# Optimization experiments

Measured on AMD Instinct MI355X. Metric: run time of the kernel, lower is better.

The kernel has to match this reference:

```python
import jax, jax.numpy as jnp
import numpy as np

NUM_EMBED = 1024
EMBED_DIM = 256
DECAY = 0.99
EPS = 1e-05
COMMIT = 0.25


def setup_inputs() -> dict:
    key = jax.random.key(0)
    k1, k2, k3 = jax.random.split(key, 3)
    z = jax.random.normal(k1, (64, 32, 32, EMBED_DIM), dtype=jnp.float32)
    lim = 1.0 / NUM_EMBED
    embeddings = jax.random.uniform(k2, (NUM_EMBED, EMBED_DIM), minval=-lim, maxval=lim, dtype=jnp.float32)
    ema_embed = jax.random.uniform(k3, (NUM_EMBED, EMBED_DIM), minval=-lim, maxval=lim, dtype=jnp.float32)
    cluster_size = jnp.zeros((NUM_EMBED,), dtype=jnp.float32)
    return {"z": z, "embeddings": embeddings, "ema_embed": ema_embed, "cluster_size": cluster_size}


def reference(z, embeddings, ema_embed, cluster_size):
    B, H, W, D = z.shape
    zf = z.reshape(-1, D)  # [N, D]
    # squared euclidean distances to codebook: [N, K]
    distances = (zf ** 2).sum(-1, keepdims=True) + (embeddings ** 2).sum(-1) - 2.0 * (zf @ embeddings.T)
    closest = jnp.argmin(distances, axis=-1)  # [N] int
    quantized_indices = closest.reshape(B, H, W)[:, None]  # [B,1,H,W]
    quantized = embeddings[closest].reshape(z.shape)  # gather instead of one-hot GEMM

    # --- training-mode EMA codebook update (buffer math, no grads) ---
    n_i = jnp.zeros((NUM_EMBED,), dtype=zf.dtype).at[closest].add(1.0)  # per-code counts
    new_cluster = cluster_size * DECAY + n_i * (1.0 - DECAY)
    dw = jnp.zeros_like(embeddings).at[closest].add(zf)  # scatter-add of assigned vectors
    new_ema = ema_embed * DECAY + dw * (1.0 - DECAY)
    n = new_cluster.sum()
    new_cluster = (new_cluster + EPS) / (n + NUM_EMBED * EPS) * n
    new_embeddings = new_ema / new_cluster[:, None]

    commitment_loss = jnp.mean((quantized - z) ** 2)
    st_quantized = z + jax.lax.stop_gradient(quantized - z)  # straight-through
    loss = commitment_loss * COMMIT
    return loss, st_quantized, quantized_indices, new_embeddings, new_cluster, new_ema
```

## Files before the change

kernel.cpp:

```cpp
#include <hip/hip_runtime.h>
#include <float.h>
#include <stdint.h>

#define K_EMB 1024
#define D_EMB 256

typedef _Float16 half8 __attribute__((ext_vector_type(8)));
typedef float f32x4_t __attribute__((ext_vector_type(4)));


__global__ void convert_e_kernel(const float* __restrict__ e, _Float16* __restrict__ ehp,
                                 float* __restrict__ t2, unsigned int* __restrict__ flag_cnt) {
  if (blockIdx.x == 0 && threadIdx.x == 0) { flag_cnt[0] = 0; flag_cnt[1] = 0; }
  int row = blockIdx.x * 4 + (threadIdx.x >> 6);
  int lane = threadIdx.x & 63;
  float4 v = ((const float4*)(e + (size_t)row * D_EMB))[lane];
  float s = v.x * v.x + v.y * v.y + v.z * v.z + v.w * v.w;
#pragma unroll
  for (int off = 32; off > 0; off >>= 1) s += __shfl_down(s, off, 64);
  if (lane == 0) t2[row] = s;
  _Float16* dst = ehp + (size_t)row * D_EMB + lane * 4;
  dst[0] = (_Float16)v.x; dst[1] = (_Float16)v.y;
  dst[2] = (_Float16)v.z; dst[3] = (_Float16)v.w;
}


#define BM 256
#define CCH 64
#define NCH (K_EMB / CCH)
#define DELTA 1.5e-4f

__launch_bounds__(512, 2)
__global__ void argmin_mfma_kernel(const float* __restrict__ z,
                                   const _Float16* __restrict__ eh,
                                   const float* __restrict__ t2,
                                   int* __restrict__ closest,
                                   float* __restrict__ idx_out,
                                   unsigned int* __restrict__ flag_cnt,
                                   unsigned int* __restrict__ flag_row,
                                   unsigned int* __restrict__ flag_cand) {
  __shared__ _Float16 ebuf[CCH * D_EMB];
  const int tid = threadIdx.x;
  const int wid = tid >> 6;
  const int lane = tid & 63;
  const int c = lane & 15, g = lane >> 4;
  const int row0 = blockIdx.x * BM + wid * 32;

  half8 A[2][8];
#pragma unroll
  for (int fr = 0; fr < 2; ++fr)
#pragma unroll
    for (int df = 0; df < 8; ++df) {
      const float* zp = z + (size_t)(row0 + fr * 16 + c) * D_EMB + df * 32 + g * 8;
      const float4 v0 = *(const float4*)zp;
      const float4 v1 = *(const float4*)(zp + 4);
      half8 h;
      h[0] = (_Float16)v0.x; h[1] = (_Float16)v0.y; h[2] = (_Float16)v0.z; h[3] = (_Float16)v0.w;
      h[4] = (_Float16)v1.x; h[5] = (_Float16)v1.y; h[6] = (_Float16)v1.z; h[7] = (_Float16)v1.w;
      A[fr][df] = h;
    }

  float m1[8], m2[8], m3[8];
  int k1[8], k2[8];
#pragma unroll
  for (int s = 0; s < 8; ++s) { m1[s] = FLT_MAX; m2[s] = FLT_MAX; m3[s] = FLT_MAX; k1[s] = 0; k2[s] = 0; }

#define INS(s, dvv, kkv)                                        \
  {                                                             \
    const float dv_ = (dvv); const int kk_ = (kkv);             \
    const bool lt1 = dv_ < m1[s], lt2 = dv_ < m2[s], lt3 = dv_ < m3[s]; \
    m3[s] = lt2 ? m2[s] : (lt3 ? dv_ : m3[s]);                  \
    m2[s] = lt1 ? m1[s] : (lt2 ? dv_ : m2[s]);                  \
    k2[s] = lt1 ? k1[s] : (lt2 ? kk_ : k2[s]);                  \
    m1[s] = lt1 ? dv_ : m1[s];                                  \
    k1[s] = lt1 ? kk_ : k1[s];                                  \
  }

  const int scode = tid >> 3;
  const int s8 = tid & 7;
  const int swz_w = (scode & 7) << 3;
  const int rswz = (c & 7) << 3;

  for (int cb = 0; cb < NCH; ++cb) {
    __syncthreads();
    {
      const _Float16* src = eh + (size_t)(cb * CCH + scode) * D_EMB + s8 * 32;
      _Float16* dst = ebuf + scode * D_EMB;
#pragma unroll
      for (int u = 0; u < 4; ++u) {
        int elem = s8 * 32 + u * 8;
        *(half8*)(dst + (elem ^ swz_w)) = *(const half8*)(src + u * 8);
      }
    }
    __syncthreads();

    f32x4_t acc[2][4];
#pragma unroll
    for (int fr = 0; fr < 2; ++fr)
#pragma unroll
      for (int fc = 0; fc < 4; ++fc) acc[fr][fc] = (f32x4_t){0.f, 0.f, 0.f, 0.f};

#pragma unroll
    for (int d = 0; d < 8; ++d) {
      half8 Bh[4];
#pragma unroll
      for (int fc = 0; fc < 4; ++fc) {
        const int elem = (d * 32 + g * 8) ^ rswz;
        Bh[fc] = *(const half8*)(ebuf + (fc * 16 + c) * D_EMB + elem);
      }
#pragma unroll
      for (int fr = 0; fr < 2; ++fr)
#pragma unroll
        for (int fc = 0; fc < 4; ++fc)
          acc[fr][fc] = __builtin_amdgcn_mfma_f32_16x16x32_f16(A[fr][d], Bh[fc], acc[fr][fc], 0, 0, 0);
    }

#pragma unroll
    for (int fc = 0; fc < 4; ++fc) {
      const int kk = cb * CCH + fc * 16 + c;
      const float t2c = t2[kk];
#pragma unroll
      for (int fr = 0; fr < 2; ++fr)
#pragma unroll
        for (int r = 0; r < 4; ++r) {
          const float dv = fmaf(-2.f, acc[fr][fc][r], t2c);
          const int s = fr * 4 + r;
          INS(s, dv, kk)
        }
    }
  }

#pragma unroll
  for (int m = 1; m <= 8; m <<= 1) {
#pragma unroll
    for (int s = 0; s < 8; ++s) {
      const float om1 = __shfl_xor(m1[s], m, 64);
      const int ok1 = __shfl_xor(k1[s], m, 64);
      const float om2 = __shfl_xor(m2[s], m, 64);
      const int ok2 = __shfl_xor(k2[s], m, 64);
      const float om3 = __shfl_xor(m3[s], m, 64);
      INS(s, om1, ok1)
      INS(s, om2, ok2)
      m3[s] = fminf(m3[s], om3);
    }
  }
#undef INS

  if (c == 0) {
#pragma unroll
    for (int s = 0; s < 8; ++s) {
      const int fr = s >> 2, r = s & 3;
      const int row = row0 + fr * 16 + g * 4 + r;
      closest[row] = k1[s];
      idx_out[row] = (float)k1[s];
      if (m2[s] - m1[s] < DELTA) {
        const unsigned int p = atomicAdd(flag_cnt, 1u);
        flag_row[p] = (unsigned int)row;
        flag_cand[p] = (unsigned int)k1[s] | ((unsigned int)k2[s] << 10) |
                       ((m3[s] - m1[s] < DELTA) ? (1u << 20) : 0u);
      }
    }
  }
}


__launch_bounds__(256, 4)
__global__ void fixup_pair_kernel(const float* __restrict__ z, const float* __restrict__ emb,
                                  const float* __restrict__ t2,
                                  const unsigned int* __restrict__ flag_cnt,
                                  const unsigned int* __restrict__ flag_row,
                                  const unsigned int* __restrict__ flag_cand,
                                  int* __restrict__ closest, float* __restrict__ idx_out,
                                  unsigned int* __restrict__ flag2_cnt,
                                  unsigned int* __restrict__ flag2) {
  const int tid = threadIdx.x;
  const int q = tid & 3;
  const unsigned int cnt = *flag_cnt;
  const unsigned int nquads = (gridDim.x * 256) >> 2;
  for (unsigned int i = (blockIdx.x * 256 + tid) >> 2; i < cnt; i += nquads) {
    const int row = (int)flag_row[i];
    const unsigned int cand = flag_cand[i];
    if ((cand >> 20) & 1u) {
      if (q == 0) {
        const unsigned int p = atomicAdd(flag2_cnt, 1u);
        flag2[p] = (unsigned int)row;
      }
      continue;
    }
    const int ka = (int)(cand & 1023u), kb = (int)((cand >> 10) & 1023u);
    const float4* zp = (const float4*)(z + (size_t)row * D_EMB) + q * 16;
    const float4* ap = (const float4*)(emb + (size_t)ka * D_EMB) + q * 16;
    const float4* bp = (const float4*)(emb + (size_t)kb * D_EMB) + q * 16;
    float s0 = 0.f, sa = 0.f, sb = 0.f;
#pragma unroll 8
    for (int u = 0; u < 16; ++u) {
      const float4 zv = zp[u], av = ap[u], bv = bp[u];
      s0 = fmaf(zv.x, zv.x, s0); s0 = fmaf(zv.y, zv.y, s0);
      s0 = fmaf(zv.z, zv.z, s0); s0 = fmaf(zv.w, zv.w, s0);
      sa = fmaf(zv.x, av.x, sa); sa = fmaf(zv.y, av.y, sa);
      sa = fmaf(zv.z, av.z, sa); sa = fmaf(zv.w, av.w, sa);
      sb = fmaf(zv.x, bv.x, sb); sb = fmaf(zv.y, bv.y, sb);
      sb = fmaf(zv.z, bv.z, sb); sb = fmaf(zv.w, bv.w, sb);
    }
#pragma unroll
    for (int m = 1; m <= 2; m <<= 1) {
      s0 += __shfl_xor(s0, m, 64);
      sa += __shfl_xor(sa, m, 64);
      sb += __shfl_xor(sb, m, 64);
    }
    if (q == 0) {
      const float da = (s0 + t2[ka]) - 2.f * sa;
      const float db = (s0 + t2[kb]) - 2.f * sb;
      int kbest = ka;
      if (db < da || (db == da && kb < ka)) kbest = kb;
      closest[row] = kbest;
      idx_out[row] = (float)kbest;
    }
  }
}


__launch_bounds__(256, 4)
__global__ void fixup_full_kernel(const float* __restrict__ z, const float* __restrict__ emb,
                                  const float* __restrict__ t2,
                                  const unsigned int* __restrict__ flag2_cnt,
                                  const unsigned int* __restrict__ flag2,
                                  int* __restrict__ closest, float* __restrict__ idx_out) {
  __shared__ float zs[D_EMB];
  __shared__ float t1s;
  __shared__ float redm[4];
  __shared__ int redk[4];
  const int tid = threadIdx.x;
  const int lane = tid & 63, wv = tid >> 6;
  const unsigned int cnt = *flag2_cnt;
  for (unsigned int j = blockIdx.x; j < cnt; j += gridDim.x) {
    __syncthreads();
    const int row = (int)flag2[j];
    if (wv == 0) {
      const float4 v = ((const float4*)(z + (size_t)row * D_EMB))[lane];
      ((float4*)zs)[lane] = v;
      float s = v.x * v.x + v.y * v.y + v.z * v.z + v.w * v.w;
#pragma unroll
      for (int off = 32; off > 0; off >>= 1) s += __shfl_down(s, off, 64);
      if (lane == 0) t1s = s;
    }
    __syncthreads();
    const float4* e0 = (const float4*)(emb + (size_t)(4 * tid + 0) * D_EMB);
    const float4* e1 = (const float4*)(emb + (size_t)(4 * tid + 1) * D_EMB);
    const float4* e2 = (const float4*)(emb + (size_t)(4 * tid + 2) * D_EMB);
    const float4* e3 = (const float4*)(emb + (size_t)(4 * tid + 3) * D_EMB);
    const float4* zp4 = (const float4*)zs;
    float a0 = 0.f, a1 = 0.f, a2 = 0.f, a3 = 0.f;
    for (int i = 0; i < 64; ++i) {
      const float4 z4 = zp4[i];
      const float4 v0 = e0[i], v1 = e1[i], v2 = e2[i], v3 = e3[i];
      a0 = fmaf(z4.x, v0.x, a0); a0 = fmaf(z4.y, v0.y, a0);
      a0 = fmaf(z4.z, v0.z, a0); a0 = fmaf(z4.w, v0.w, a0);
      a1 = fmaf(z4.x, v1.x, a1); a1 = fmaf(z4.y, v1.y, a1);
      a1 = fmaf(z4.z, v1.z, a1); a1 = fmaf(z4.w, v1.w, a1);
      a2 = fmaf(z4.x, v2.x, a2); a2 = fmaf(z4.y, v2.y, a2);
      a2 = fmaf(z4.z, v2.z, a2); a2 = fmaf(z4.w, v2.w, a2);
      a3 = fmaf(z4.x, v3.x, a3); a3 = fmaf(z4.y, v3.y, a3);
      a3 = fmaf(z4.z, v3.z, a3); a3 = fmaf(z4.w, v3.w, a3);
    }
    const float t1v = t1s;
    float best = FLT_MAX;
    int bk = 0x7fffffff;
    const float dvs[4] = {(t1v + t2[4 * tid + 0]) - 2.f * a0,
                          (t1v + t2[4 * tid + 1]) - 2.f * a1,
                          (t1v + t2[4 * tid + 2]) - 2.f * a2,
                          (t1v + t2[4 * tid + 3]) - 2.f * a3};
#pragma unroll
    for (int cc = 0; cc < 4; ++cc) {
      const int k = 4 * tid + cc;
      if (dvs[cc] < best) { best = dvs[cc]; bk = k; }
    }
#pragma unroll
    for (int m = 1; m <= 32; m <<= 1) {
      const float ob = __shfl_xor(best, m, 64);
      const int ok = __shfl_xor(bk, m, 64);
      if (ob < best || (ob == best && ok < bk)) { best = ob; bk = ok; }
    }
    if (lane == 0) { redm[wv] = best; redk[wv] = bk; }
    __syncthreads();
    if (tid == 0) {
      float b = redm[0];
      int k = redk[0];
#pragma unroll
      for (int w = 1; w < 4; ++w)
        if (redm[w] < b || (redm[w] == b && redk[w] < k)) { b = redm[w]; k = redk[w]; }
      closest[row] = k;
      idx_out[row] = (float)k;
    }
  }
}


__global__ void hist1_kernel(const int* __restrict__ closest, unsigned int* __restrict__ rank,
                             unsigned int* __restrict__ blockhist) {
  __shared__ unsigned int lh[K_EMB];
  const int t = threadIdx.x;
  lh[t] = 0;
  __syncthreads();
  const int row = blockIdx.x * 1024 + t;
  rank[row] = atomicAdd(&lh[closest[row]], 1u);
  __syncthreads();
  blockhist[blockIdx.x * K_EMB + t] = lh[t];
}

__global__ void hist2_kernel(unsigned int* __restrict__ blockhist, const float* __restrict__ cs,
                             unsigned int* __restrict__ base, float* __restrict__ newc,
                             float* __restrict__ o_ncl, int nblocks) {
  __shared__ unsigned int sc[K_EMB];
  __shared__ float fr[K_EMB];
  const int bin = threadIdx.x;
  unsigned int s = 0;
  for (int b = 0; b < nblocks; ++b) {
    const unsigned int v = blockhist[b * K_EMB + bin];
    blockhist[b * K_EMB + bin] = s;
    s += v;
  }
  sc[bin] = s;
  __syncthreads();
  for (int off = 1; off < K_EMB; off <<= 1) {
    const unsigned int t = (bin >= off) ? sc[bin - off] : 0u;
    __syncthreads();
    sc[bin] += t;
    __syncthreads();
  }
  base[bin] = sc[bin] - s;
  const float pre = cs[bin] * 0.99f + (float)s * (float)(1.0 - 0.99);
  fr[bin] = pre;
  __syncthreads();
  for (int st = 512; st > 0; st >>= 1) {
    if (bin < st) fr[bin] += fr[bin + st];
    __syncthreads();
  }
  const float n = fr[0];
  const float ncl = (pre + 1e-5f) / (n + (float)(K_EMB * 1e-5)) * n;
  newc[bin] = ncl;
  o_ncl[bin] = ncl;
}

__global__ void hist3_kernel(const int* __restrict__ closest, const unsigned int* __restrict__ rank,
                             const unsigned int* __restrict__ blockhist,
                             const unsigned int* __restrict__ base,
                             unsigned int* __restrict__ sorted) {
  const int t = threadIdx.x;
  const int row = blockIdx.x * 1024 + t;
  const int k = closest[row];
  sorted[base[k] + blockhist[blockIdx.x * K_EMB + k] + rank[row]] = (unsigned int)row;
}


__global__ void dwsum_kernel(const float* __restrict__ z, const unsigned int* __restrict__ sorted,
                             const unsigned int* __restrict__ base, const float* __restrict__ ema,
                             const float* __restrict__ newc, const float* __restrict__ emb,
                             float* __restrict__ o_st, float* __restrict__ o_nema,
                             float* __restrict__ o_nemb, float* __restrict__ loss_part, int N) {
  const int k = blockIdx.x;
  const int lane = threadIdx.x & 63, wv = threadIdx.x >> 6;
  const unsigned int b0 = base[k];
  const unsigned int b1 = (k == K_EMB - 1) ? (unsigned int)N : base[k + 1];
  const float4 ev = ((const float4*)(emb + (size_t)k * D_EMB))[lane];
  float4 acc = {0.f, 0.f, 0.f, 0.f};
  float ls = 0.f;
  for (unsigned int j = b0 + wv; j < b1; j += 4) {
    const unsigned int row = sorted[j];
    const float4 zv = ((const float4*)(z + (size_t)row * D_EMB))[lane];
    const float dx = ev.x - zv.x, dy = ev.y - zv.y, dz = ev.z - zv.z, dww = ev.w - zv.w;
    float* sp = o_st + (size_t)row * D_EMB + lane * 4;
    sp[0] = zv.x + dx; sp[1] = zv.y + dy; sp[2] = zv.z + dz; sp[3] = zv.w + dww;
    ls = fmaf(dx, dx, ls); ls = fmaf(dy, dy, ls);
    ls = fmaf(dz, dz, ls); ls = fmaf(dww, dww, ls);
    acc.x += zv.x; acc.y += zv.y; acc.z += zv.z; acc.w += zv.w;
  }
  __shared__ float4 red[256];
  __shared__ float lred[256];
  red[threadIdx.x] = acc;
  lred[threadIdx.x] = ls;
  __syncthreads();
  for (int s = 128; s > 0; s >>= 1) {
    if (threadIdx.x < s) lred[threadIdx.x] += lred[threadIdx.x + s];
    __syncthreads();
  }
  if (threadIdx.x == 0) loss_part[k] = lred[0];
  if (wv == 0) {
    const float4 a1 = red[64 + lane], a2 = red[128 + lane], a3 = red[192 + lane];
    acc = red[lane];
    acc.x += a1.x + a2.x + a3.x;
    acc.y += a1.y + a2.y + a3.y;
    acc.z += a1.z + a2.z + a3.z;
    acc.w += a1.w + a2.w + a3.w;
    const float4 emv = ((const float4*)ema)[k * 64 + lane];
    const float nc = newc[k];
    const int off = k * D_EMB + lane * 4;
    float ne;
    ne = emv.x * 0.99f + acc.x * (float)(1.0 - 0.99); o_nema[off + 0] = ne; o_nemb[off + 0] = ne / nc;
    ne = emv.y * 0.99f + acc.y * (float)(1.0 - 0.99); o_nema[off + 1] = ne; o_nemb[off + 1] = ne / nc;
    ne = emv.z * 0.99f + acc.z * (float)(1.0 - 0.99); o_nema[off + 2] = ne; o_nemb[off + 2] = ne / nc;
    ne = emv.w * 0.99f + acc.w * (float)(1.0 - 0.99); o_nema[off + 3] = ne; o_nemb[off + 3] = ne / nc;
  }
}

__global__ void loss_final_kernel(const float* __restrict__ loss_part,
                                  float* __restrict__ o_loss, int nrows) {
  const int i = threadIdx.x;
  __shared__ double dred[1024];
  dred[i] = (double)loss_part[i];
  __syncthreads();
  for (int s = 512; s > 0; s >>= 1) {
    if (i < s) dred[i] += dred[i + s];
    __syncthreads();
  }
  if (i == 0) o_loss[0] = (float)(0.25 * (dred[0] / ((double)nrows * (double)D_EMB)));
}


extern "C" void kernel_launch(void* const* d_in, const int* in_sizes, int n_in,
                              void* d_out, int out_size, void* d_ws, size_t ws_size,
                              hipStream_t stream) {
  const float* z = (const float*)d_in[0];
  const float* emb = (const float*)d_in[1];
  const float* ema = (const float*)d_in[2];
  const float* cs = (const float*)d_in[3];
  const int N = in_sizes[0] / D_EMB;
  const int NB = N / 1024;

  float* out = (float*)d_out;
  float* o_loss = out;
  float* o_st = out + 1;
  float* o_idx = o_st + (size_t)N * D_EMB;
  float* o_nemb = o_idx + N;
  float* o_ncl = o_nemb + (size_t)K_EMB * D_EMB;
  float* o_nema = o_ncl + K_EMB;

  float* ws = (float*)d_ws;
  float* t2 = ws;
  float* newc = t2 + K_EMB;
  float* loss_part = newc + K_EMB;
  unsigned int* flag_cnt = (unsigned int*)(loss_part + K_EMB);
  unsigned int* basep = flag_cnt + 4;
  _Float16* ehp = (_Float16*)(basep + K_EMB);
  int* closest = (int*)(ehp + (size_t)K_EMB * D_EMB);
  unsigned int* flag_row = (unsigned int*)(closest + N);
  unsigned int* flag_cand = flag_row + N;
  unsigned int* sorted = flag_cand + N;
  unsigned int* flag2 = sorted + N;

  unsigned int* rank = flag_row;
  unsigned int* blockhist = flag_cand;
  unsigned int* flag2_cnt = flag_cnt + 1;

  convert_e_kernel<<<K_EMB / 4, 256, 0, stream>>>(emb, ehp, t2, flag_cnt);
  argmin_mfma_kernel<<<N / BM, 512, 0, stream>>>(z, ehp, t2, closest, o_idx,
                                                 flag_cnt, flag_row, flag_cand);
  fixup_pair_kernel<<<128, 256, 0, stream>>>(z, emb, t2, flag_cnt, flag_row, flag_cand,
                                             closest, o_idx, flag2_cnt, flag2);
  fixup_full_kernel<<<128, 256, 0, stream>>>(z, emb, t2, flag2_cnt, flag2, closest, o_idx);
  hist1_kernel<<<NB, 1024, 0, stream>>>(closest, rank, blockhist);
  hist2_kernel<<<1, 1024, 0, stream>>>(blockhist, cs, basep, newc, o_ncl, NB);
  hist3_kernel<<<NB, 1024, 0, stream>>>(closest, rank, blockhist, basep, sorted);
  dwsum_kernel<<<K_EMB, 256, 0, stream>>>(z, sorted, basep, ema, newc, emb,
                                          o_st, o_nema, o_nemb, loss_part, N);
  loss_final_kernel<<<1, 1024, 0, stream>>>(loss_part, o_loss, N);
}
```

Measured before the change: 195.4 us.

## Double-buffer codebook chunks in LDS and use med3 for top-3 insert

```diff
diff --git a/kernel.cpp b/kernel.cpp
--- a/kernel.cpp
+++ b/kernel.cpp
@@ -39,7 +39,7 @@
                                    unsigned int* __restrict__ flag_cnt,
                                    unsigned int* __restrict__ flag_row,
                                    unsigned int* __restrict__ flag_cand) {
-  __shared__ _Float16 ebuf[CCH * D_EMB];
+  __shared__ _Float16 ebuf[2 * CCH * D_EMB];
   const int tid = threadIdx.x;
   const int wid = tid >> 6;
   const int lane = tid & 63;
@@ -68,11 +68,13 @@
 #define INS(s, dvv, kkv)                                        \
   {                                                             \
     const float dv_ = (dvv); const int kk_ = (kkv);             \
-    const bool lt1 = dv_ < m1[s], lt2 = dv_ < m2[s], lt3 = dv_ < m3[s]; \
-    m3[s] = lt2 ? m2[s] : (lt3 ? dv_ : m3[s]);                  \
-    m2[s] = lt1 ? m1[s] : (lt2 ? dv_ : m2[s]);                  \
+    const bool lt1 = dv_ < m1[s];                               \
+    const bool lt2 = dv_ < m2[s];                               \
+    m3[s] = __builtin_amdgcn_fmed3f(m2[s], m3[s], dv_);         \
+    const float nm2 = __builtin_amdgcn_fmed3f(m1[s], m2[s], dv_); \
     k2[s] = lt1 ? k1[s] : (lt2 ? kk_ : k2[s]);                  \
-    m1[s] = lt1 ? dv_ : m1[s];                                  \
+    m2[s] = nm2;                                                \
+    m1[s] = fminf(m1[s], dv_);                                  \
     k1[s] = lt1 ? kk_ : k1[s];                                  \
   }
 
@@ -81,19 +83,30 @@
   const int swz_w = (scode & 7) << 3;
   const int rswz = (c & 7) << 3;
 
+  half8 st[4];
+  {
+    const _Float16* src = eh + (size_t)scode * D_EMB + s8 * 8;
+#pragma unroll
+    for (int u = 0; u < 4; ++u) st[u] = *(const half8*)(src + u * 64);
+    _Float16* dst = ebuf + scode * D_EMB;
+#pragma unroll
+    for (int u = 0; u < 4; ++u) {
+      const int elem = (s8 * 8 + u * 64) ^ swz_w;
+      *(half8*)(dst + elem) = st[u];
+    }
+  }
+
+  int cur = 0;
   for (int cb = 0; cb < NCH; ++cb) {
     __syncthreads();
-    {
-      const _Float16* src = eh + (size_t)(cb * CCH + scode) * D_EMB + s8 * 32;
-      _Float16* dst = ebuf + scode * D_EMB;
-#pragma unroll
-      for (int u = 0; u < 4; ++u) {
-        int elem = s8 * 32 + u * 8;
-        *(half8*)(dst + (elem ^ swz_w)) = *(const half8*)(src + u * 8);
-      }
-    }
-    __syncthreads();
-
+
+    if (cb + 1 < NCH) {
+      const _Float16* src = eh + (size_t)((cb + 1) * CCH + scode) * D_EMB + s8 * 8;
+#pragma unroll
+      for (int u = 0; u < 4; ++u) st[u] = *(const half8*)(src + u * 64);
+    }
+
+    const _Float16* rb = ebuf + cur * (CCH * D_EMB);
     f32x4_t acc[2][4];
 #pragma unroll
     for (int fr = 0; fr < 2; ++fr)
@@ -106,13 +119,22 @@
 #pragma unroll
       for (int fc = 0; fc < 4; ++fc) {
         const int elem = (d * 32 + g * 8) ^ rswz;
-        Bh[fc] = *(const half8*)(ebuf + (fc * 16 + c) * D_EMB + elem);
+        Bh[fc] = *(const half8*)(rb + (fc * 16 + c) * D_EMB + elem);
       }
 #pragma unroll
       for (int fr = 0; fr < 2; ++fr)
 #pragma unroll
         for (int fc = 0; fc < 4; ++fc)
           acc[fr][fc] = __builtin_amdgcn_mfma_f32_16x16x32_f16(A[fr][d], Bh[fc], acc[fr][fc], 0, 0, 0);
+    }
+
+    if (cb + 1 < NCH) {
+      _Float16* dst = ebuf + (cur ^ 1) * (CCH * D_EMB) + scode * D_EMB;
+#pragma unroll
+      for (int u = 0; u < 4; ++u) {
+        const int elem = (s8 * 8 + u * 64) ^ swz_w;
+        *(half8*)(dst + elem) = st[u];
+      }
     }
 
 #pragma unroll
@@ -128,6 +150,7 @@
           INS(s, dv, kk)
         }
     }
+    cur ^= 1;
   }
 
 #pragma unroll
```

After: 199.3 us. No clear change (+2.0%).
